# Optimization experiments

Hardware: AMD Instinct MI355X
Metric: run time of the kernel (lower is better)

Reference implementation:

```python
import jax, jax.numpy as jnp
import numpy as np
import math

KV_STRIDE = 2
Q_STRIDE = 1
WAVE_LEN = 1000.0
POS_MAG = 1.0


def _pos_embed(h, w, h_kv, w_kv, q_stride, kv_stride, feat_dim):
    # Sinusoidal relative-position embeddings, matching get_position_embedding.
    h_idx = jnp.arange(h, dtype=jnp.float32) * q_stride
    w_idx = jnp.arange(w, dtype=jnp.float32) * q_stride
    h_kv_idx = jnp.arange(h_kv, dtype=jnp.float32) * kv_stride
    w_kv_idx = jnp.arange(w_kv, dtype=jnp.float32) * kv_stride
    h_diff = (h_idx[:, None] - h_kv_idx[None, :]) * POS_MAG  # (h, h_kv)
    w_diff = (w_idx[:, None] - w_kv_idx[None, :]) * POS_MAG  # (w, w_kv)
    feat_range = jnp.arange(feat_dim // 4, dtype=jnp.float32)
    dim_mat = WAVE_LEN ** (4.0 / feat_dim * feat_range)  # (feat_dim//4,)
    wd = w_diff[:, :, None] / dim_mat  # (w, w_kv, F)
    hd = h_diff[:, :, None] / dim_mat  # (h, h_kv, F)
    emb_x = jnp.concatenate([jnp.sin(wd), jnp.cos(wd)], axis=2)  # (w, w_kv, feat_dim//2)
    emb_y = jnp.concatenate([jnp.sin(hd), jnp.cos(hd)], axis=2)  # (h, h_kv, feat_dim//2)
    return emb_x, emb_y


def setup_inputs() -> dict:
    key = jax.random.key(0)
    ks = jax.random.split(key, 11)
    C = 288
    s = 1.0 / math.sqrt(C)
    return {
        'x_input': jax.random.normal(ks[0], (2, C, 64, 64), jnp.float32),
        'Wq': jax.random.normal(ks[1], (C, C), jnp.float32) * s,
        'Wk': jax.random.normal(ks[2], (C, C), jnp.float32) * s,
        'Wv': jax.random.normal(ks[3], (C, C), jnp.float32) * s,
        'Wx': jax.random.normal(ks[4], (C, C // 2), jnp.float32) * s,
        'Wy': jax.random.normal(ks[5], (C, C // 2), jnp.float32) * s,
        'Wproj': jax.random.normal(ks[6], (C, C), jnp.float32) * s,
        'bproj': jax.random.normal(ks[7], (C,), jnp.float32) * 0.02,
        'Wc': jax.random.normal(ks[8], (9, C), jnp.float32) * s,
        'bc': jax.random.normal(ks[9], (9,), jnp.float32) * 0.02,
        'gamma': jax.random.normal(ks[10], (1,), jnp.float32),
    }


def reference(x_input, Wq, Wk, Wv, Wx, Wy, Wproj, bproj, Wc, bc, gamma):
    M = Wc.shape[0]                       # num_mixtures
    n, C, h, w = x_input.shape
    d = Wq.shape[0] // M                  # qk_embed_dim (== v_dim)
    x_q = x_input                         # q_stride == 1
    x_kv = x_input[:, :, ::KV_STRIDE, ::KV_STRIDE]  # AvgPool2d(k=1, stride=2)
    h_kv, w_kv = x_kv.shape[2], x_kv.shape[3]

    # 1x1 convs as channel GEMMs
    q = jnp.einsum('nchw,oc->nohw', x_q, Wq).reshape(n, M, d, h * w)
    q = q.transpose(0, 1, 3, 2)                                    # (n,M,hw,d)
    k = jnp.einsum('nchw,oc->nohw', x_kv, Wk).reshape(n, M, d, h_kv * w_kv)

    emb_x, emb_y = _pos_embed(h, w, h_kv, w_kv, Q_STRIDE, KV_STRIDE, C)
    inv_sqrt2 = 1.0 / math.sqrt(2.0)
    pf_x = (emb_x @ Wx.T).reshape(w, w_kv, M, d).transpose(2, 0, 1, 3) * inv_sqrt2  # (M,w,w_kv,d)
    pf_y = (emb_y @ Wy.T).reshape(h, h_kv, M, d).transpose(2, 0, 1, 3) * inv_sqrt2  # (M,h,h_kv,d)

    energy = jnp.matmul(q, k).reshape(n, M, h, w, h_kv, w_kv)
    q5 = q.reshape(n, M, h, w, d)
    e_x = jnp.einsum('nmhwd,mwvd->nmhwv', q5, pf_x)  # (n,M,h,w,w_kv)
    e_y = jnp.einsum('nmhwd,mhud->nmhwu', q5, pf_y)  # (n,M,h,w,h_kv)
    energy = energy + e_x[:, :, :, :, None, :] + e_y[:, :, :, :, :, None]
    energy = energy.reshape(n, M, h * w, h_kv * w_kv)
    attn = jax.nn.softmax(energy, axis=3)

    # Learned per-mixture gating from mean query context
    context = q.transpose(0, 1, 3, 2).reshape(n, M * d, h * w).mean(axis=2)  # (n, M*d)
    mix_w = jax.nn.softmax(context @ Wc.T + bc, axis=1)                      # (n, M)
    attn = jnp.sum(attn * mix_w[:, :, None, None], axis=1)                   # (n,hw,hw_kv)

    v = jnp.einsum('nchw,oc->nohw', x_kv, Wv).reshape(n, M * d, h_kv * w_kv)
    v = v.transpose(0, 2, 1)                                                 # (n,hw_kv,M*d)
    out = jnp.matmul(attn, v).transpose(0, 2, 1).reshape(n, M * d, h, w)
    out = jnp.einsum('nchw,oc->nohw', out, Wproj) + bproj[None, :, None, None]
    return gamma[0] * out + x_input
```

## Files before the change

### kernel.cpp

```cpp
#include <hip/hip_runtime.h>
#include <math.h>

#define NB     2
#define CDIM   288
#define HW     4096
#define PKV    1024
#define MHEAD  9
#define DHEAD  32

typedef __attribute__((ext_vector_type(8))) short bf16x8;
typedef __attribute__((ext_vector_type(4))) float f32x4;

#if __has_builtin(__builtin_amdgcn_exp2f)
#define EXP2(x) __builtin_amdgcn_exp2f(x)
#else
#define EXP2(x) exp2f(x)
#endif

__device__ inline unsigned short f2bf(float x) {
    unsigned int u = __float_as_uint(x);
    u = (u + 0x7fffu + ((u >> 16) & 1u)) >> 16;
    return (unsigned short)u;
}


__global__ __launch_bounds__(256) void prep(const float* __restrict__ X,
        const float* __restrict__ Wq, const float* __restrict__ Wk,
        const float* __restrict__ Wv, const float* __restrict__ Wproj,
        const float* __restrict__ Wx, const float* __restrict__ Wy,
        unsigned short* __restrict__ XF, unsigned short* __restrict__ WFq,
        unsigned short* __restrict__ WFk, unsigned short* __restrict__ WFv,
        unsigned short* __restrict__ WFp, float* __restrict__ WTx,
        float* __restrict__ WTy, float* __restrict__ MX) {
    __shared__ float t32[32][133];
    __shared__ float t16[16][17];
    __shared__ float red[4];
    int b = blockIdx.x;
    int tid = threadIdx.x;
    if (b < 576) {
        int bx = b % 32, by = (b / 32) % 9, n = b / 288;
        int j0 = bx * 128, c0 = by * 32;
        int c = tid >> 3, f = tid & 7;
        const float* src = &X[((size_t)n * CDIM + c0 + c) * HW + j0];
#pragma unroll
        for (int l = 0; l < 4; ++l) {
            float4 v = *(const float4*)&src[(f + l * 8) * 4];
            *(float4*)&t32[c][(f + l * 8) * 4] = v;
        }
        __syncthreads();
        int cc = c0 >> 5;
#pragma unroll
        for (int l = 0; l < 4; ++l) {
            int g = l * 256 + tid;
            int s = g >> 7;
            int w = g & 127;
            int lane = w >> 1, e0 = (w & 1) * 4;
            int jl = s * 16 + (lane & 15);
            int cb = (lane >> 4) * 8 + e0;
            unsigned int w0 = f2bf(t32[cb + 0][jl]) | ((unsigned int)f2bf(t32[cb + 1][jl]) << 16);
            unsigned int w1 = f2bf(t32[cb + 2][jl]) | ((unsigned int)f2bf(t32[cb + 3][jl]) << 16);
            int jt = (j0 >> 4) + s;
            unsigned short* O = XF + (size_t)n * HW * CDIM + ((size_t)jt * 9 + cc) * 512 + lane * 8 + e0;
            uint2 pk = { w0, w1 };
            *(uint2*)O = pk;
        }
    } else if (b < 900) {
        int u = b - 576;
        int bx = u % 9, by = (u / 9) % 18, bz = u / 162;
        const float* W = bz ? Wy : Wx;
        float* WT      = bz ? WTy : WTx;
        int f0 = bx * 16, o0 = by * 16;
        int tx = tid & 15, ty = tid >> 4;
        t16[ty][tx] = W[(o0 + ty) * 144 + f0 + tx];
        __syncthreads();
        WT[(f0 + ty) * 288 + o0 + tx] = t16[tx][ty];
    } else if (b < 1062) {
        int t = b - 900;
        int sub = tid >> 6, lane = tid & 63;
        int ot = t / 9, cc = t % 9;
        const float* W = (sub == 0) ? Wq : (sub == 1) ? Wk : (sub == 2) ? Wv : Wproj;
        unsigned short* O = ((sub == 0) ? WFq : (sub == 1) ? WFk : (sub == 2) ? WFv : WFp)
                            + (size_t)t * 512;
        int o  = ot * 16 + (lane & 15);
        int c0 = cc * 32 + (lane >> 4) * 8;
        const float* src = W + (size_t)o * CDIM + c0;
        float4 f0 = *(const float4*)src, f1 = *(const float4*)(src + 4);
        unsigned int v0 = f2bf(f0.x) | ((unsigned int)f2bf(f0.y) << 16);
        unsigned int v1 = f2bf(f0.z) | ((unsigned int)f2bf(f0.w) << 16);
        unsigned int v2 = f2bf(f1.x) | ((unsigned int)f2bf(f1.y) << 16);
        unsigned int v3 = f2bf(f1.z) | ((unsigned int)f2bf(f1.w) << 16);
        uint4 pk = { v0, v1, v2, v3 };
        *(uint4*)(O + lane * 8) = pk;
    } else {
        int bid = b - 1062;
        const float* xr = X + (size_t)bid * HW;
        float s = 0.f;
        for (int j = tid; j < HW; j += 256) s += xr[j];
        for (int off = 32; off > 0; off >>= 1) s += __shfl_xor(s, off, 64);
        if ((tid & 63) == 0) red[tid >> 6] = s;
        __syncthreads();
        if (tid == 0) MX[bid] = (red[0] + red[1] + red[2] + red[3]) * (1.f / 4096.f);
    }
}

__global__ __launch_bounds__(256) void mid(
        const float* __restrict__ WTx, const float* __restrict__ WTy,
        unsigned short* __restrict__ FXb, unsigned short* __restrict__ FYb,
        const float* __restrict__ Wq, const float* __restrict__ MX,
        const float* __restrict__ Wc, const float* __restrict__ bc,
        float* __restrict__ MIXW,
        const unsigned short* __restrict__ WFq, const unsigned short* __restrict__ WFk,
        const unsigned short* __restrict__ WFv, const unsigned short* __restrict__ XF,
        unsigned short* __restrict__ Qf, unsigned short* __restrict__ KF,
        unsigned short* __restrict__ VF) {
    __shared__ float emb[144];
    __shared__ float ctx_s[NB * CDIM];
    __shared__ float lg[18];
    __shared__ __attribute__((aligned(16))) unsigned short tr[4][32][40];
    int b = blockIdx.x;
    int tid = threadIdx.x;

    if (b < 252) {
        int axis = b / 126;
        int dif  = b % 126;
        float diff = (float)(dif - 62);
        if (tid < 72) {
            float dm = expf(6.9077552789821368f * ((float)tid * (1.f / 72.f)));
            float t  = diff / dm;
            emb[tid]      = sinf(t);
            emb[72 + tid] = cosf(t);
        }
        __syncthreads();
        const float* WT = axis ? WTy : WTx;
        unsigned short* F = axis ? FYb : FXb;
        for (int o = tid; o < CDIM; o += 256) {
            float s = 0.f;
#pragma unroll 8
            for (int f = 0; f < 144; ++f) s += emb[f] * WT[f * 288 + o];
            int m = o >> 5, d = o & 31;
            F[(size_t)(m * 8 + (dif >> 4)) * 512 + ((dif & 15) + 16 * (d >> 3)) * 8 + (d & 7)]
                = f2bf(s * 0.70710678118654752f);
        }
    } else if (b == 252) {
        for (int idx = tid; idx < 1152; idx += 256) {
            int d = idx & 31, rr = (idx >> 5) & 1, mm = (idx >> 6) % 9, ax = idx / 576;
            int dif = 126 + rr;
            unsigned short* F = ax ? FYb : FXb;
            F[(size_t)(mm * 8 + 7) * 512 + ((dif & 15) + 16 * (d >> 3)) * 8 + (d & 7)] = 0;
        }
        for (int p = tid; p < NB * CDIM; p += 256) {
            int n = p / CDIM, o = p % CDIM;
            const float* wr = Wq + (size_t)o * CDIM;
            const float* mx = MX + n * CDIM;
            float s = 0.f;
            for (int c = 0; c < CDIM; c += 4) {
                float4 w4 = *(const float4*)&wr[c];
                float4 m4 = *(const float4*)&mx[c];
                s += w4.x * m4.x + w4.y * m4.y + w4.z * m4.z + w4.w * m4.w;
            }
            ctx_s[p] = s;
        }
        __syncthreads();
        if (tid < 18) {
            int n = tid / 9, j = tid % 9;
            float s = bc[j];
            for (int o = 0; o < CDIM; ++o) s += ctx_s[n * CDIM + o] * Wc[j * CDIM + o];
            lg[tid] = s;
        }
        __syncthreads();
        if (tid < 2) {
            float mx = -1e30f;
            for (int j = 0; j < 9; ++j) mx = fmaxf(mx, lg[tid * 9 + j]);
            float e[9], sm = 0.f;
            for (int j = 0; j < 9; ++j) { e[j] = __expf(lg[tid * 9 + j] - mx); sm += e[j]; }
            for (int j = 0; j < 9; ++j) MIXW[tid * 9 + j] = e[j] / sm;
        }
    } else {
        int bx = b - 253;
        int gx = bx % 40;
        int m  = (bx / 40) % 9;
        int n  = bx / 360;
        int wv = tid >> 6, lane = tid & 63;
        int lq = lane & 15, quad = lane >> 4;
        if (gx < 32) {
            int j0 = gx * 128;
            int jw = j0 + wv * 32;
            const unsigned short* Wb = WFq + ((size_t)(m * 2) * 9) * 512 + lane * 8;
            const unsigned short* Xb = XF + (size_t)n * HW * CDIM + ((size_t)(jw >> 4) * 9) * 512 + lane * 8;
            f32x4 acc[2][2] = {};
#pragma unroll
            for (int cc = 0; cc < 9; ++cc) {
                bf16x8 a0 = *(const bf16x8*)(Wb + (size_t)cc * 512);
                bf16x8 a1 = *(const bf16x8*)(Wb + (size_t)(9 + cc) * 512);
                bf16x8 b0 = *(const bf16x8*)(Xb + (size_t)cc * 512);
                bf16x8 b1 = *(const bf16x8*)(Xb + (size_t)(9 + cc) * 512);
                acc[0][0] = __builtin_amdgcn_mfma_f32_16x16x32_bf16(a0, b0, acc[0][0], 0, 0, 0);
                acc[0][1] = __builtin_amdgcn_mfma_f32_16x16x32_bf16(a0, b1, acc[0][1], 0, 0, 0);
                acc[1][0] = __builtin_amdgcn_mfma_f32_16x16x32_bf16(a1, b0, acc[1][0], 0, 0, 0);
                acc[1][1] = __builtin_amdgcn_mfma_f32_16x16x32_bf16(a1, b1, acc[1][1], 0, 0, 0);
            }
#pragma unroll
            for (int oi = 0; oi < 2; ++oi)
#pragma unroll
                for (int ji = 0; ji < 2; ++ji)
#pragma unroll
                    for (int r = 0; r < 4; ++r)
                        tr[wv][ji * 16 + lq][oi * 16 + quad * 4 + r]
                            = f2bf(1.4426950408889634f * acc[oi][ji][r]);
            int jl = lane & 31, half = lane >> 5;
            bf16x8 v0 = *(const bf16x8*)&tr[wv][jl][half * 16];
            bf16x8 v1 = *(const bf16x8*)&tr[wv][jl][half * 16 + 8];
            unsigned short* Qm = Qf + ((size_t)(n * MHEAD + m) * HW + jw + jl) * 32 + half * 16;
            *(bf16x8*)Qm = v0;
            *(bf16x8*)(Qm + 8) = v1;
        } else {
            int p0 = (gx - 32) * 128;
            int pw = p0 + wv * 32;
            const unsigned short* XFn = XF + (size_t)n * HW * CDIM;
            size_t bidx[2];
#pragma unroll
            for (int pi = 0; pi < 2; ++pi) {
                int p   = pw + pi * 16 + lq;
                int pos = ((p >> 5) << 7) + ((p & 31) << 1);
                bidx[pi] = ((size_t)(pos >> 4) * 9) * 512 + ((pos & 15) + 16 * quad) * 8;
            }
            const unsigned short* Wkb = WFk + ((size_t)(m * 2) * 9) * 512 + lane * 8;
            const unsigned short* Wvb = WFv + ((size_t)(m * 2) * 9) * 512 + lane * 8;
            f32x4 ak[2][2] = {}, av[2][2] = {};
#pragma unroll
            for (int cc = 0; cc < 9; ++cc) {
                bf16x8 a0k = *(const bf16x8*)(Wkb + (size_t)cc * 512);
                bf16x8 a1k = *(const bf16x8*)(Wkb + (size_t)(9 + cc) * 512);
                bf16x8 a0v = *(const bf16x8*)(Wvb + (size_t)cc * 512);
                bf16x8 a1v = *(const bf16x8*)(Wvb + (size_t)(9 + cc) * 512);
                bf16x8 b0  = *(const bf16x8*)(XFn + bidx[0] + (size_t)cc * 512);
                bf16x8 b1  = *(const bf16x8*)(XFn + bidx[1] + (size_t)cc * 512);
                ak[0][0] = __builtin_amdgcn_mfma_f32_16x16x32_bf16(a0k, b0, ak[0][0], 0, 0, 0);
                ak[0][1] = __builtin_amdgcn_mfma_f32_16x16x32_bf16(a0k, b1, ak[0][1], 0, 0, 0);
                ak[1][0] = __builtin_amdgcn_mfma_f32_16x16x32_bf16(a1k, b0, ak[1][0], 0, 0, 0);
                ak[1][1] = __builtin_amdgcn_mfma_f32_16x16x32_bf16(a1k, b1, ak[1][1], 0, 0, 0);
                av[0][0] = __builtin_amdgcn_mfma_f32_16x16x32_bf16(a0v, b0, av[0][0], 0, 0, 0);
                av[0][1] = __builtin_amdgcn_mfma_f32_16x16x32_bf16(a0v, b1, av[0][1], 0, 0, 0);
                av[1][0] = __builtin_amdgcn_mfma_f32_16x16x32_bf16(a1v, b0, av[1][0], 0, 0, 0);
                av[1][1] = __builtin_amdgcn_mfma_f32_16x16x32_bf16(a1v, b1, av[1][1], 0, 0, 0);
            }
#pragma unroll
            for (int oi = 0; oi < 2; ++oi)
#pragma unroll
                for (int pi = 0; pi < 2; ++pi)
#pragma unroll
                    for (int r = 0; r < 4; ++r)
                        tr[wv][pi * 16 + lq][oi * 16 + quad * 4 + r] = f2bf(ak[oi][pi][r]);
            unsigned short* KFm = KF + (size_t)(n * MHEAD + m) * (PKV * 32);
#pragma unroll
            for (int pi = 0; pi < 2; ++pi) {
                bf16x8 v = *(const bf16x8*)&tr[wv][pi * 16 + lq][quad * 8];
                *(bf16x8*)(KFm + (size_t)((pw >> 4) + pi) * 512 + lane * 8) = v;
            }
#pragma unroll
            for (int oi = 0; oi < 2; ++oi)
#pragma unroll
                for (int pi = 0; pi < 2; ++pi)
#pragma unroll
                    for (int r = 0; r < 4; ++r)
                        tr[wv][oi * 16 + quad * 4 + r][pi * 16 + lq] = f2bf(av[oi][pi][r]);
            unsigned short* VFn = VF + (size_t)n * CDIM * PKV;
#pragma unroll
            for (int oi = 0; oi < 2; ++oi) {
                bf16x8 v = *(const bf16x8*)&tr[wv][oi * 16 + lq][quad * 8];
                *(bf16x8*)(VFn + (size_t)((m * 2 + oi) * 32 + (pw >> 5)) * 512 + lane * 8) = v;
            }
        }
    }
}

__global__ __launch_bounds__(512, 4) void attn_fused6(
        const unsigned short* __restrict__ Qf, const unsigned short* __restrict__ KF,
        const unsigned short* __restrict__ VF, const unsigned short* __restrict__ WFp,
        const unsigned short* __restrict__ FXb, const unsigned short* __restrict__ FYb,
        const float* __restrict__ MIXW, const float* __restrict__ bproj,
        const float* __restrict__ x, const float* __restrict__ gamma,
        float* __restrict__ OUT) {
    int n    = blockIdx.x >> 8;
    int i0   = (blockIdx.x & 255) * 16;
    int tid  = threadIdx.x;
    int wv   = tid >> 6;
    int lane = tid & 63;
    int lq   = lane & 15;
    int quad = lane >> 4;

    int bx_t = (i0 & 63) >> 4;
    int h    = i0 >> 6;
    int by_t = h >> 4;
    int dh   = h & 15;

    __shared__ __attribute__((aligned(16))) float Rx_s[2][16][82];
    __shared__ __attribute__((aligned(16))) float Ry_s[2][16][82];
    __shared__ __attribute__((aligned(16))) float ws_s[2][16][8];
    __shared__ __attribute__((aligned(16))) unsigned short tr[16][1032];
    unsigned short (*Mt)[296] = (unsigned short (*)[296])&Rx_s[0][0][0];

    float mixed[8][4];
#pragma unroll
    for (int t = 0; t < 8; ++t)
#pragma unroll
        for (int j = 0; j < 4; ++j) mixed[t][j] = 0.f;

    auto r_phase = [&](int mm, bf16x8 af) {
        int pp = mm & 1;
        if (wv < 5) {
            bf16x8 bR = *(const bf16x8*)(FXb + (size_t)(mm * 8 + bx_t + wv) * 512 + lane * 8);
            f32x4 r = (f32x4){0.f, 0.f, 0.f, 0.f};
            r = __builtin_amdgcn_mfma_f32_16x16x32_bf16(af, bR, r, 0, 0, 0);
#pragma unroll
            for (int reg = 0; reg < 4; ++reg)
                Rx_s[pp][quad * 4 + reg][wv * 16 + lq] = r[reg];
        } else {
            bf16x8 bR = *(const bf16x8*)(FYb + (size_t)(mm * 8 + by_t + (wv - 5)) * 512 + lane * 8);
            f32x4 r = (f32x4){0.f, 0.f, 0.f, 0.f};
            r = __builtin_amdgcn_mfma_f32_16x16x32_bf16(af, bR, r, 0, 0, 0);
#pragma unroll
            for (int reg = 0; reg < 4; ++reg)
                Ry_s[pp][quad * 4 + reg][(wv - 5) * 16 + lq] = r[reg];
        }
        if (wv < 2) {
            bf16x8 bR = *(const bf16x8*)(FYb + (size_t)(mm * 8 + by_t + 3 + wv) * 512 + lane * 8);
            f32x4 r = (f32x4){0.f, 0.f, 0.f, 0.f};
            r = __builtin_amdgcn_mfma_f32_16x16x32_bf16(af, bR, r, 0, 0, 0);
#pragma unroll
            for (int reg = 0; reg < 4; ++reg)
                Ry_s[pp][quad * 4 + reg][(3 + wv) * 16 + lq] = r[reg];
        }
    };

    bf16x8 af_cur = *(const bf16x8*)(Qf + (((size_t)n * MHEAD) * HW + i0 + lq) * 32 + quad * 8);
    r_phase(0, af_cur);
    __syncthreads();

#pragma unroll 1
    for (int m = 0; m < MHEAD; ++m) {
        const unsigned short* KmF = KF + (size_t)(n * MHEAD + m) * (PKV * 32);
        bf16x8 kf[8];
#pragma unroll
        for (int t = 0; t < 8; ++t)
            kf[t] = *(const bf16x8*)(KmF + (size_t)(wv * 8 + t) * 512 + lane * 8);

        bf16x8 af_nxt = af_cur;
        __builtin_amdgcn_s_setprio(1);
        if (m + 1 < MHEAD) {
            af_nxt = *(const bf16x8*)(Qf + (((size_t)(n * MHEAD + m + 1)) * HW + i0 + lq) * 32 + quad * 8);
            r_phase(m + 1, af_nxt);
        }
        f32x4 acc[8];
#pragma unroll
        for (int t = 0; t < 8; ++t) {
            f32x4 z = (f32x4){0.f, 0.f, 0.f, 0.f};
            acc[t] = __builtin_amdgcn_mfma_f32_16x16x32_bf16(af_cur, kf[t], z, 0, 0, 0);
        }
        __builtin_amdgcn_s_setprio(0);

        int par = m & 1;
        float exA[4], exB[4];
#pragma unroll
        for (int j = 0; j < 4; ++j) {
            int q = quad * 4 + j;
            exA[j] = Rx_s[par][q][q + 62 - 2 * lq];
            exB[j] = Rx_s[par][q][q + 30 - 2 * lq];
        }
        float rs[4] = {0.f, 0.f, 0.f, 0.f};
#pragma unroll
        for (int tp = 0; tp < 4; ++tp) {
            int u = wv * 4 + tp;
            float ey[4];
#pragma unroll
            for (int j = 0; j < 4; ++j) ey[j] = Ry_s[par][quad * 4 + j][dh + 62 - 2 * u];
#pragma unroll
            for (int half = 0; half < 2; ++half) {
                int t = tp * 2 + half;
#pragma unroll
                for (int j = 0; j < 4; ++j) {
                    float e = EXP2(acc[t][j] + (half ? exB[j] : exA[j]) + ey[j]);
                    rs[j] += e;
                    acc[t][j] = e;
                }
            }
        }
#pragma unroll
        for (int j = 0; j < 4; ++j) {
            rs[j] += __shfl_xor(rs[j], 1, 64);
            rs[j] += __shfl_xor(rs[j], 2, 64);
            rs[j] += __shfl_xor(rs[j], 4, 64);
            rs[j] += __shfl_xor(rs[j], 8, 64);
        }
        if (lq == 0) {
#pragma unroll
            for (int j = 0; j < 4; ++j) ws_s[par][quad * 4 + j][wv] = rs[j];
        }
        __syncthreads();

        {
            float wm = MIXW[n * MHEAD + m];
#pragma unroll
            for (int j = 0; j < 4; ++j) {
                int q = quad * 4 + j;
                float4 w0 = *(const float4*)&ws_s[par][q][0];
                float4 w1 = *(const float4*)&ws_s[par][q][4];
                float lt = (w0.x + w0.y) + (w0.z + w0.w) + (w1.x + w1.y) + (w1.z + w1.w);
                float fct = wm / lt;
#pragma unroll
                for (int t = 0; t < 8; ++t) mixed[t][j] += acc[t][j] * fct;
            }
        }
        __builtin_amdgcn_sched_barrier(0);
        af_cur = af_nxt;
    }

#pragma unroll
    for (int t = 0; t < 8; ++t)
#pragma unroll
        for (int j = 0; j < 4; ++j)
            tr[quad * 4 + j][wv * 128 + t * 16 + lq] = f2bf(mixed[t][j]);
    __syncthreads();

    const unsigned short* VFn = VF + (size_t)n * CDIM * PKV;
    f32x4 accpv[3];
#pragma unroll
    for (int idx = 0; idx < 3; ++idx) accpv[idx] = (f32x4){0.f, 0.f, 0.f, 0.f};
#pragma unroll 4
    for (int pc = 0; pc < 32; ++pc) {
        bf16x8 pf = *(const bf16x8*)&tr[lq][pc * 32 + quad * 8];
#pragma unroll
        for (int idx = 0; idx < 3; ++idx) {
            int ot = wv + idx * 8;
            if (ot < 18) {
                bf16x8 vf = *(const bf16x8*)(VFn + (size_t)(ot * 32 + pc) * 512 + lane * 8);
                accpv[idx] = __builtin_amdgcn_mfma_f32_16x16x32_bf16(pf, vf, accpv[idx], 0, 0, 0);
            }
        }
    }
#pragma unroll
    for (int idx = 0; idx < 3; ++idx) {
        int ot = wv + idx * 8;
        if (ot < 18) {
#pragma unroll
            for (int r = 0; r < 4; ++r)
                Mt[quad * 4 + r][ot * 16 + lq] = f2bf(accpv[idx][r]);
        }
    }
    __syncthreads();

    float g = gamma[0];
#pragma unroll
    for (int idx = 0; idx < 3; ++idx) {
        int ot = wv + idx * 8;
        if (ot >= 18) continue;
        f32x4 acco = (f32x4){0.f, 0.f, 0.f, 0.f};
#pragma unroll
        for (int cc = 0; cc < 9; ++cc) {
            bf16x8 af = *(const bf16x8*)(WFp + (size_t)(ot * 9 + cc) * 512 + lane * 8);
            bf16x8 bfm = *(const bf16x8*)&Mt[lq][cc * 32 + quad * 8];
            acco = __builtin_amdgcn_mfma_f32_16x16x32_bf16(af, bfm, acco, 0, 0, 0);
        }
#pragma unroll
        for (int r = 0; r < 4; ++r) {
            int o = ot * 16 + quad * 4 + r;
            size_t id = ((size_t)(n * CDIM) + o) * HW + i0 + lq;
            OUT[id] = g * (acco[r] + bproj[o]) + x[id];
        }
    }
}

extern "C" void kernel_launch(void* const* d_in, const int* in_sizes, int n_in,
                              void* d_out, int out_size, void* d_ws, size_t ws_size,
                              hipStream_t stream) {
    const float* x     = (const float*)d_in[0];
    const float* Wq    = (const float*)d_in[1];
    const float* Wk    = (const float*)d_in[2];
    const float* Wv    = (const float*)d_in[3];
    const float* Wx    = (const float*)d_in[4];
    const float* Wy    = (const float*)d_in[5];
    const float* Wproj = (const float*)d_in[6];
    const float* bproj = (const float*)d_in[7];
    const float* Wc    = (const float*)d_in[8];
    const float* bc    = (const float*)d_in[9];
    const float* gamma = (const float*)d_in[10];
    float* out = (float*)d_out;

    float* ws = (float*)d_ws;
    size_t off = 0;
    unsigned short* Qf  = (unsigned short*)(ws + off); off += (size_t)NB * MHEAD * HW * 32 / 2;
    unsigned short* KF  = (unsigned short*)(ws + off); off += (size_t)NB * MHEAD * PKV * 32 / 2;
    unsigned short* VF  = (unsigned short*)(ws + off); off += (size_t)NB * CDIM * PKV / 2;
    unsigned short* WFq = (unsigned short*)(ws + off); off += (size_t)CDIM * CDIM / 2;
    unsigned short* WFk = (unsigned short*)(ws + off); off += (size_t)CDIM * CDIM / 2;
    unsigned short* WFv = (unsigned short*)(ws + off); off += (size_t)CDIM * CDIM / 2;
    unsigned short* WFp = (unsigned short*)(ws + off); off += (size_t)CDIM * CDIM / 2;
    unsigned short* XF  = (unsigned short*)(ws + off); off += (size_t)NB * HW * CDIM / 2;
    float* WTx  = ws + off; off += 144 * 288;
    float* WTy  = ws + off; off += 144 * 288;
    unsigned short* FXb = (unsigned short*)(ws + off); off += (size_t)MHEAD * 8 * 512 / 2;
    unsigned short* FYb = (unsigned short*)(ws + off); off += (size_t)MHEAD * 8 * 512 / 2;
    float* MX   = ws + off; off += NB * CDIM;
    float* MIXW = ws + off; off += 32;

    prep<<<1638, 256, 0, stream>>>(x, Wq, Wk, Wv, Wproj, Wx, Wy,
                                   XF, WFq, WFk, WFv, WFp, WTx, WTy, MX);
    mid<<<973, 256, 0, stream>>>(WTx, WTy, FXb, FYb, Wq, MX, Wc, bc, MIXW,
                                 WFq, WFk, WFv, XF, Qf, KF, VF);
    attn_fused6<<<NB * HW / 16, 512, 0, stream>>>(Qf, KF, VF, WFp, FXb, FYb, MIXW,
                                                  bproj, x, gamma, out);
}
```

Before: 177.2 us.

## Process two 16-query tiles per 1024-thread block to share V loads

The fused attention kernel now handles 32 queries per block with 1024 threads, running two independent 16-query halves through the energy/softmax phase. In the P·V stage each wave loads a V fragment once and applies it to both query tiles, halving global V traffic per query, and work is redistributed so 16 waves cover the 18 output tiles. Shared memory is consolidated into one aliased buffer to fit the larger tile. The cost is fewer blocks, a bigger block with more barrier contention, and launch_bounds(1024,4) register pressure that may cause spills.

```diff
diff --git a/kernel.cpp b/kernel.cpp
--- a/kernel.cpp
+++ b/kernel.cpp
@@ -274,31 +274,34 @@
     }
 }
 
-__global__ __launch_bounds__(512, 4) void attn_fused6(
+__global__ __launch_bounds__(1024, 4) void attn_fused7(
         const unsigned short* __restrict__ Qf, const unsigned short* __restrict__ KF,
         const unsigned short* __restrict__ VF, const unsigned short* __restrict__ WFp,
         const unsigned short* __restrict__ FXb, const unsigned short* __restrict__ FYb,
         const float* __restrict__ MIXW, const float* __restrict__ bproj,
         const float* __restrict__ x, const float* __restrict__ gamma,
         float* __restrict__ OUT) {
-    int n    = blockIdx.x >> 8;
-    int i0   = (blockIdx.x & 255) * 16;
+    int n    = blockIdx.x >> 7;
+    int i0   = (blockIdx.x & 127) * 32;
     int tid  = threadIdx.x;
     int wv   = tid >> 6;
+    int ti   = wv >> 3;
+    int w8   = wv & 7;
     int lane = tid & 63;
     int lq   = lane & 15;
     int quad = lane >> 4;
-
-    int bx_t = (i0 & 63) >> 4;
-    int h    = i0 >> 6;
-    int by_t = h >> 4;
-    int dh   = h & 15;
-
-    __shared__ __attribute__((aligned(16))) float Rx_s[2][16][82];
-    __shared__ __attribute__((aligned(16))) float Ry_s[2][16][82];
-    __shared__ __attribute__((aligned(16))) float ws_s[2][16][8];
-    __shared__ __attribute__((aligned(16))) unsigned short tr[16][1032];
-    unsigned short (*Mt)[296] = (unsigned short (*)[296])&Rx_s[0][0][0];
+    int it0  = i0 + ti * 16;
+
+    int bx_t = (it0 & 63) >> 4;
+    int hh   = i0 >> 6;
+    int by_t = hh >> 4;
+    int dh   = hh & 15;
+
+    __shared__ __attribute__((aligned(16))) unsigned short tr[32][1032];
+    float (*Rx_s)[2][16][82] = reinterpret_cast<float (*)[2][16][82]>((char*)&tr[0][0]);
+    float (*Ry_s)[2][16][82] = reinterpret_cast<float (*)[2][16][82]>((char*)&tr[0][0] + 20992);
+    float (*ws_s)[2][16][8]  = reinterpret_cast<float (*)[2][16][8]>((char*)&tr[0][0] + 41984);
+    unsigned short (*Mt)[296] = reinterpret_cast<unsigned short (*)[296]>(&tr[0][0]);
 
     float mixed[8][4];
 #pragma unroll
@@ -308,32 +311,32 @@
 
     auto r_phase = [&](int mm, bf16x8 af) {
         int pp = mm & 1;
-        if (wv < 5) {
-            bf16x8 bR = *(const bf16x8*)(FXb + (size_t)(mm * 8 + bx_t + wv) * 512 + lane * 8);
+        if (w8 < 5) {
+            bf16x8 bR = *(const bf16x8*)(FXb + (size_t)(mm * 8 + bx_t + w8) * 512 + lane * 8);
             f32x4 r = (f32x4){0.f, 0.f, 0.f, 0.f};
             r = __builtin_amdgcn_mfma_f32_16x16x32_bf16(af, bR, r, 0, 0, 0);
 #pragma unroll
             for (int reg = 0; reg < 4; ++reg)
-                Rx_s[pp][quad * 4 + reg][wv * 16 + lq] = r[reg];
+                Rx_s[pp][ti][quad * 4 + reg][w8 * 16 + lq] = r[reg];
         } else {
-            bf16x8 bR = *(const bf16x8*)(FYb + (size_t)(mm * 8 + by_t + (wv - 5)) * 512 + lane * 8);
+            bf16x8 bR = *(const bf16x8*)(FYb + (size_t)(mm * 8 + by_t + (w8 - 5)) * 512 + lane * 8);
             f32x4 r = (f32x4){0.f, 0.f, 0.f, 0.f};
             r = __builtin_amdgcn_mfma_f32_16x16x32_bf16(af, bR, r, 0, 0, 0);
 #pragma unroll
             for (int reg = 0; reg < 4; ++reg)
-                Ry_s[pp][quad * 4 + reg][(wv - 5) * 16 + lq] = r[reg];
-        }
-        if (wv < 2) {
-            bf16x8 bR = *(const bf16x8*)(FYb + (size_t)(mm * 8 + by_t + 3 + wv) * 512 + lane * 8);
+                Ry_s[pp][ti][quad * 4 + reg][(w8 - 5) * 16 + lq] = r[reg];
+        }
+        if (w8 < 2) {
+            bf16x8 bR = *(const bf16x8*)(FYb + (size_t)(mm * 8 + by_t + 3 + w8) * 512 + lane * 8);
             f32x4 r = (f32x4){0.f, 0.f, 0.f, 0.f};
             r = __builtin_amdgcn_mfma_f32_16x16x32_bf16(af, bR, r, 0, 0, 0);
 #pragma unroll
             for (int reg = 0; reg < 4; ++reg)
-                Ry_s[pp][quad * 4 + reg][(3 + wv) * 16 + lq] = r[reg];
+                Ry_s[pp][ti][quad * 4 + reg][(3 + w8) * 16 + lq] = r[reg];
         }
     };
 
-    bf16x8 af_cur = *(const bf16x8*)(Qf + (((size_t)n * MHEAD) * HW + i0 + lq) * 32 + quad * 8);
+    bf16x8 af_cur = *(const bf16x8*)(Qf + (((size_t)n * MHEAD) * HW + it0 + lq) * 32 + quad * 8);
     r_phase(0, af_cur);
     __syncthreads();
 
@@ -343,12 +346,12 @@
         bf16x8 kf[8];
 #pragma unroll
         for (int t = 0; t < 8; ++t)
-            kf[t] = *(const bf16x8*)(KmF + (size_t)(wv * 8 + t) * 512 + lane * 8);
+            kf[t] = *(const bf16x8*)(KmF + (size_t)(w8 * 8 + t) * 512 + lane * 8);
 
         bf16x8 af_nxt = af_cur;
         __builtin_amdgcn_s_setprio(1);
         if (m + 1 < MHEAD) {
-            af_nxt = *(const bf16x8*)(Qf + (((size_t)(n * MHEAD + m + 1)) * HW + i0 + lq) * 32 + quad * 8);
+            af_nxt = *(const bf16x8*)(Qf + (((size_t)(n * MHEAD + m + 1)) * HW + it0 + lq) * 32 + quad * 8);
             r_phase(m + 1, af_nxt);
         }
         f32x4 acc[8];
@@ -364,16 +367,16 @@
 #pragma unroll
         for (int j = 0; j < 4; ++j) {
             int q = quad * 4 + j;
-            exA[j] = Rx_s[par][q][q + 62 - 2 * lq];
-            exB[j] = Rx_s[par][q][q + 30 - 2 * lq];
+            exA[j] = Rx_s[par][ti][q][q + 62 - 2 * lq];
+            exB[j] = Rx_s[par][ti][q][q + 30 - 2 * lq];
         }
         float rs[4] = {0.f, 0.f, 0.f, 0.f};
 #pragma unroll
         for (int tp = 0; tp < 4; ++tp) {
-            int u = wv * 4 + tp;
+            int u = w8 * 4 + tp;
             float ey[4];
 #pragma unroll
-            for (int j = 0; j < 4; ++j) ey[j] = Ry_s[par][quad * 4 + j][dh + 62 - 2 * u];
+            for (int j = 0; j < 4; ++j) ey[j] = Ry_s[par][ti][quad * 4 + j][dh + 62 - 2 * u];
 #pragma unroll
             for (int half = 0; half < 2; ++half) {
                 int t = tp * 2 + half;
@@ -394,7 +397,7 @@
         }
         if (lq == 0) {
 #pragma unroll
-            for (int j = 0; j < 4; ++j) ws_s[par][quad * 4 + j][wv] = rs[j];
+            for (int j = 0; j < 4; ++j) ws_s[par][ti][quad * 4 + j][w8] = rs[j];
         }
         __syncthreads();
 
@@ -403,8 +406,8 @@
 #pragma unroll
             for (int j = 0; j < 4; ++j) {
                 int q = quad * 4 + j;
-                float4 w0 = *(const float4*)&ws_s[par][q][0];
-                float4 w1 = *(const float4*)&ws_s[par][q][4];
+                float4 w0 = *(const float4*)&ws_s[par][ti][q][0];
+                float4 w1 = *(const float4*)&ws_s[par][ti][q][4];
                 float lt = (w0.x + w0.y) + (w0.z + w0.w) + (w1.x + w1.y) + (w1.z + w1.w);
                 float fct = wm / lt;
 #pragma unroll
@@ -415,56 +418,65 @@
         af_cur = af_nxt;
     }
 
+    __syncthreads();
+
 #pragma unroll
     for (int t = 0; t < 8; ++t)
 #pragma unroll
         for (int j = 0; j < 4; ++j)
-            tr[quad * 4 + j][wv * 128 + t * 16 + lq] = f2bf(mixed[t][j]);
+            tr[ti * 16 + quad * 4 + j][w8 * 128 + t * 16 + lq] = f2bf(mixed[t][j]);
     __syncthreads();
 
     const unsigned short* VFn = VF + (size_t)n * CDIM * PKV;
-    f32x4 accpv[3];
-#pragma unroll
-    for (int idx = 0; idx < 3; ++idx) accpv[idx] = (f32x4){0.f, 0.f, 0.f, 0.f};
+    f32x4 accpv[2][2];
+#pragma unroll
+    for (int oi = 0; oi < 2; ++oi)
+#pragma unroll
+        for (int t2 = 0; t2 < 2; ++t2) accpv[oi][t2] = (f32x4){0.f, 0.f, 0.f, 0.f};
+    bool has2 = (wv < 2);
 #pragma unroll 4
     for (int pc = 0; pc < 32; ++pc) {
-        bf16x8 pf = *(const bf16x8*)&tr[lq][pc * 32 + quad * 8];
-#pragma unroll
-        for (int idx = 0; idx < 3; ++idx) {
-            int ot = wv + idx * 8;
-            if (ot < 18) {
-                bf16x8 vf = *(const bf16x8*)(VFn + (size_t)(ot * 32 + pc) * 512 + lane * 8);
-                accpv[idx] = __builtin_amdgcn_mfma_f32_16x16x32_bf16(pf, vf, accpv[idx], 0, 0, 0);
-            }
-        }
-    }
-#pragma unroll
-    for (int idx = 0; idx < 3; ++idx) {
-        int ot = wv + idx * 8;
-        if (ot < 18) {
-#pragma unroll
-            for (int r = 0; r < 4; ++r)
-                Mt[quad * 4 + r][ot * 16 + lq] = f2bf(accpv[idx][r]);
+        bf16x8 pf0 = *(const bf16x8*)&tr[lq][pc * 32 + quad * 8];
+        bf16x8 pf1 = *(const bf16x8*)&tr[16 + lq][pc * 32 + quad * 8];
+        bf16x8 vf0 = *(const bf16x8*)(VFn + (size_t)(wv * 32 + pc) * 512 + lane * 8);
+        accpv[0][0] = __builtin_amdgcn_mfma_f32_16x16x32_bf16(pf0, vf0, accpv[0][0], 0, 0, 0);
+        accpv[0][1] = __builtin_amdgcn_mfma_f32_16x16x32_bf16(pf1, vf0, accpv[0][1], 0, 0, 0);
+        if (has2) {
+            bf16x8 vf1 = *(const bf16x8*)(VFn + (size_t)((wv + 16) * 32 + pc) * 512 + lane * 8);
+            accpv[1][0] = __builtin_amdgcn_mfma_f32_16x16x32_bf16(pf0, vf1, accpv[1][0], 0, 0, 0);
+            accpv[1][1] = __builtin_amdgcn_mfma_f32_16x16x32_bf16(pf1, vf1, accpv[1][1], 0, 0, 0);
         }
     }
     __syncthreads();
 
+#pragma unroll
+    for (int oi = 0; oi < 2; ++oi) {
+        if (oi == 1 && !has2) continue;
+        int ot = wv + oi * 16;
+#pragma unroll
+        for (int t2 = 0; t2 < 2; ++t2)
+#pragma unroll
+            for (int r = 0; r < 4; ++r)
+                Mt[t2 * 16 + quad * 4 + r][ot * 16 + lq] = f2bf(accpv[oi][t2][r]);
+    }
+    __syncthreads();
+
     float g = gamma[0];
 #pragma unroll
     for (int idx = 0; idx < 3; ++idx) {
-        int ot = wv + idx * 8;
+        int ot = w8 + idx * 8;
         if (ot >= 18) continue;
         f32x4 acco = (f32x4){0.f, 0.f, 0.f, 0.f};
 #pragma unroll
         for (int cc = 0; cc < 9; ++cc) {
             bf16x8 af = *(const bf16x8*)(WFp + (size_t)(ot * 9 + cc) * 512 + lane * 8);
-            bf16x8 bfm = *(const bf16x8*)&Mt[lq][cc * 32 + quad * 8];
+            bf16x8 bfm = *(const bf16x8*)&Mt[ti * 16 + lq][cc * 32 + quad * 8];
             acco = __builtin_amdgcn_mfma_f32_16x16x32_bf16(af, bfm, acco, 0, 0, 0);
         }
 #pragma unroll
         for (int r = 0; r < 4; ++r) {
             int o = ot * 16 + quad * 4 + r;
-            size_t id = ((size_t)(n * CDIM) + o) * HW + i0 + lq;
+            size_t id = ((size_t)(n * CDIM) + o) * HW + it0 + lq;
             OUT[id] = g * (acco[r] + bproj[o]) + x[id];
         }
     }
@@ -507,6 +519,6 @@
                                    XF, WFq, WFk, WFv, WFp, WTx, WTy, MX);
     mid<<<973, 256, 0, stream>>>(WTx, WTy, FXb, FYb, Wq, MX, Wc, bc, MIXW,
                                  WFq, WFk, WFv, XF, Qf, KF, VF);
-    attn_fused6<<<NB * HW / 16, 512, 0, stream>>>(Qf, KF, VF, WFp, FXb, FYb, MIXW,
-                                                  bproj, x, gamma, out);
+    attn_fused7<<<NB * HW / 32, 1024, 0, stream>>>(Qf, KF, VF, WFp, FXb, FYb, MIXW,
+                                                   bproj, x, gamma, out);
 }
```

Result: no change. 174.3 us (-1.6%).
